# Kernel optimization log

Measured on AMD Instinct MI355X. Metric: run time of the kernel, lower is better.

Reference implementation:

```python
import jax, jax.numpy as jnp
import numpy as np

B, T, C, H, W = 1, 8, 128, 64, 64
F = 64  # num_feat


def setup_inputs() -> dict:
    key = jax.random.key(0)
    ks = jax.random.split(key, 8)
    return {
        "input1": jax.random.normal(ks[0], (B, T, C, H, W), jnp.float32),
        "input2": jax.random.normal(ks[1], (B, T, C, H, W), jnp.float32),
        "W1": jax.random.normal(ks[2], (F, C), jnp.float32) * 0.05,
        "b1": jax.random.normal(ks[3], (F,), jnp.float32) * 0.05,
        "W2": jax.random.normal(ks[4], (F, C), jnp.float32) * 0.05,
        "b2": jax.random.normal(ks[5], (F,), jnp.float32) * 0.05,
        "W3": jax.random.normal(ks[6], (F, C), jnp.float32) * 0.05,
        "b3": jax.random.normal(ks[7], (F,), jnp.float32) * 0.05,
    }


def reference(input1, input2, W1, b1, W2, b2, W3, b3):
    # act == 0 (ReLU branch). Conv1d(kernel=1) == per-position linear projection.
    b, t, c, h, w = input1.shape
    n = h * w
    x1 = input1.reshape(b, t, c, n)  # matches transpose(1,2).reshape then frame slice
    x2 = input2.reshape(b, t, c, n)
    q = jnp.einsum('fc,btcn->btnf', W1, x1) + b1          # [B,T,N,F]
    k = jnp.einsum('fc,btcn->btnf', W2, x2) + b2          # [B,T,N,F]
    g = jnp.einsum('fc,btcn->btnf', W3, x1) + b3          # [B,T,N,F]
    scores = jax.nn.relu(jnp.einsum('btnf,btmf->btnm', q, k))  # [B,T,N,N]
    out = jnp.einsum('btnm,btmf->btnf', scores, g)        # [B,T,N,F]
    # view([B,H,W,F]).permute(0,3,1,2), stacked over T -> [B,T,F,H,W]
    return out.reshape(b, t, h, w, -1).transpose(0, 1, 4, 2, 3)
```

## Files before the change

### kernel.cpp

```cpp
#include <hip/hip_runtime.h>
#include <hip/hip_bf16.h>

constexpr int T = 8;
constexpr int C = 128;
constexpr int N = 4096;
constexpr int F = 64;

typedef __bf16 bf16x8 __attribute__((ext_vector_type(8)));
typedef __bf16 bf16x4 __attribute__((ext_vector_type(4)));
typedef float  f32x4  __attribute__((ext_vector_type(4)));

__global__ __launch_bounds__(256) void proj_kernel(
    const float* __restrict__ x1, const float* __restrict__ x2,
    const float* __restrict__ W1, const float* __restrict__ b1,
    const float* __restrict__ W2, const float* __restrict__ b2,
    const float* __restrict__ W3, const float* __restrict__ b3,
    __bf16* __restrict__ Qb, __bf16* __restrict__ Kb, __bf16* __restrict__ Gw,
    float* __restrict__ out)
{
    const int t   = blockIdx.x >> 6;
    const int nb  = blockIdx.x & 63;
    const int tid = threadIdx.x, wave = tid >> 6, lane = tid & 63;
    const int quad = lane >> 4, l16 = lane & 15;
    const int nw = nb * 64 + wave * 16;

    {
        f32x4* o4 = (f32x4*)out + (size_t)blockIdx.x * 1024;
#pragma unroll
        for (int i = 0; i < 4; ++i) o4[i * 256 + tid] = (f32x4){0.f, 0.f, 0.f, 0.f};
    }

    bf16x8 xf1[4], xf2[4];
#pragma unroll
    for (int cc = 0; cc < 4; ++cc) {
#pragma unroll
        for (int j = 0; j < 8; ++j) {
            size_t off = ((size_t)t * C + cc * 32 + quad * 8 + j) * (size_t)N + nw + l16;
            xf1[cc][j] = (__bf16)x1[off];
            xf2[cc][j] = (__bf16)x2[off];
        }
    }

    const float* Ws[3] = {W1, W2, W3};
    const float* bs[3] = {b1, b2, b3};

#pragma unroll
    for (int p = 0; p < 3; ++p) {
        const float* W    = Ws[p];
        const float* bias = bs[p];
#pragma unroll
        for (int fb = 0; fb < 4; ++fb) {
            f32x4 acc = (f32x4){0.f, 0.f, 0.f, 0.f};
#pragma unroll
            for (int cc = 0; cc < 4; ++cc) {
                const f32x4* wp = (const f32x4*)&W[(fb * 16 + l16) * C + cc * 32 + quad * 8];
                f32x4 w0 = wp[0], w1 = wp[1];
                bf16x8 wf;
                wf[0] = (__bf16)w0[0]; wf[1] = (__bf16)w0[1];
                wf[2] = (__bf16)w0[2]; wf[3] = (__bf16)w0[3];
                wf[4] = (__bf16)w1[0]; wf[5] = (__bf16)w1[1];
                wf[6] = (__bf16)w1[2]; wf[7] = (__bf16)w1[3];
                bf16x8 xb = (p == 1) ? xf2[cc] : xf1[cc];
                acc = __builtin_amdgcn_mfma_f32_16x16x32_bf16(wf, xb, acc, 0, 0, 0);
            }
            if (p < 2) {
                __bf16* O = p ? Kb : Qb;
                bf16x4 ov;
#pragma unroll
                for (int r = 0; r < 4; ++r)
                    ov[r] = (__bf16)(acc[r] + bias[fb * 16 + quad * 4 + r]);
                *(bf16x4*)&O[((size_t)t * N + nw + l16) * F + fb * 16 + quad * 4] = ov;
            } else {
#pragma unroll
                for (int r = 0; r < 4; ++r) {
                    int f = fb * 16 + quad * 4 + r;
                    Gw[((size_t)t * F + f) * (size_t)N + nw + l16] = (__bf16)(acc[r] + bias[f]);
                }
            }
        }
    }
}

constexpr int KSPLIT = 4;

__global__ __launch_bounds__(256) void attn_kernel(
    const __bf16* __restrict__ Qb, const __bf16* __restrict__ Kb,
    const __bf16* __restrict__ Gw, float* __restrict__ out)
{
    const int ks = blockIdx.x & (KSPLIT - 1);
    const int qb = (blockIdx.x / KSPLIT) & 15;
    const int t  = blockIdx.x >> 6;
    const int q0 = qb * 256;

    constexpr int KS = 72;
    __shared__ __bf16 Kt[64 * KS];
    __shared__ __bf16 Gt[64 * KS];
    __shared__ __bf16 Sb[256 * KS];

    const int tid = threadIdx.x, wave = tid >> 6, lane = tid & 63;
    const int quad = lane >> 4, l16 = lane & 15;

    bf16x8 qf[4][2];
#pragma unroll
    for (int qg = 0; qg < 4; ++qg) {
        const __bf16* qrow = &Qb[((size_t)t * N + q0 + wave * 64 + qg * 16 + l16) * F];
        qf[qg][0] = *(const bf16x8*)&qrow[quad * 8];
        qf[qg][1] = *(const bf16x8*)&qrow[32 + quad * 8];
    }

    f32x4 oacc[4][4];
#pragma unroll
    for (int ft = 0; ft < 4; ++ft)
#pragma unroll
        for (int qg = 0; qg < 4; ++qg) oacc[ft][qg] = (f32x4){0.f, 0.f, 0.f, 0.f};

    const int kb_lo = ks * (N / 64 / KSPLIT);
    const int kb_hi = kb_lo + (N / 64 / KSPLIT);

    const int r8a = tid >> 3,          c8a = (tid & 7) * 8;
    const int r8b = (tid + 256) >> 3,  c8b = c8a;

    bf16x8 kv0, kv1, gv0, gv1;
    {
        const int k0 = kb_lo * 64;
        kv0 = *(const bf16x8*)&Kb[((size_t)t * N + k0 + r8a) * F + c8a];
        kv1 = *(const bf16x8*)&Kb[((size_t)t * N + k0 + r8b) * F + c8b];
        gv0 = *(const bf16x8*)&Gw[((size_t)t * F + r8a) * (size_t)N + k0 + c8a];
        gv1 = *(const bf16x8*)&Gw[((size_t)t * F + r8b) * (size_t)N + k0 + c8b];
    }

    for (int kb = kb_lo; kb < kb_hi; ++kb) {
        __syncthreads();
        *(bf16x8*)&Kt[r8a * KS + c8a] = kv0;
        *(bf16x8*)&Kt[r8b * KS + c8b] = kv1;
        *(bf16x8*)&Gt[r8a * KS + c8a] = gv0;
        *(bf16x8*)&Gt[r8b * KS + c8b] = gv1;
        __syncthreads();

        if (kb + 1 < kb_hi) {
            const int k0 = (kb + 1) * 64;
            kv0 = *(const bf16x8*)&Kb[((size_t)t * N + k0 + r8a) * F + c8a];
            kv1 = *(const bf16x8*)&Kb[((size_t)t * N + k0 + r8b) * F + c8b];
            gv0 = *(const bf16x8*)&Gw[((size_t)t * F + r8a) * (size_t)N + k0 + c8a];
            gv1 = *(const bf16x8*)&Gw[((size_t)t * F + r8b) * (size_t)N + k0 + c8b];
        }

#pragma unroll
        for (int nt = 0; nt < 4; ++nt) {
            bf16x8 k0f = *(const bf16x8*)&Kt[(nt * 16 + l16) * KS + quad * 8];
            bf16x8 k1f = *(const bf16x8*)&Kt[(nt * 16 + l16) * KS + 32 + quad * 8];
#pragma unroll
            for (int qg = 0; qg < 4; ++qg) {
                f32x4 s = (f32x4){0.f, 0.f, 0.f, 0.f};
                s = __builtin_amdgcn_mfma_f32_16x16x32_bf16(k0f, qf[qg][0], s, 0, 0, 0);
                s = __builtin_amdgcn_mfma_f32_16x16x32_bf16(k1f, qf[qg][1], s, 0, 0, 0);
                bf16x4 sp;
#pragma unroll
                for (int r = 0; r < 4; ++r) sp[r] = (__bf16)fmaxf(s[r], 0.f);
                *(bf16x4*)&Sb[(wave * 64 + qg * 16 + l16) * KS + nt * 16 + quad * 4] = sp;
            }
        }

        bf16x8 sf[4][2];
#pragma unroll
        for (int qg = 0; qg < 4; ++qg) {
            const __bf16* srow = &Sb[(wave * 64 + qg * 16 + l16) * KS];
            sf[qg][0] = *(const bf16x8*)&srow[quad * 8];
            sf[qg][1] = *(const bf16x8*)&srow[32 + quad * 8];
        }
#pragma unroll
        for (int ft = 0; ft < 4; ++ft) {
            bf16x8 g0 = *(const bf16x8*)&Gt[(ft * 16 + l16) * KS + quad * 8];
            bf16x8 g1 = *(const bf16x8*)&Gt[(ft * 16 + l16) * KS + 32 + quad * 8];
#pragma unroll
            for (int qg = 0; qg < 4; ++qg) {
                oacc[ft][qg] = __builtin_amdgcn_mfma_f32_16x16x32_bf16(g0, sf[qg][0], oacc[ft][qg], 0, 0, 0);
                oacc[ft][qg] = __builtin_amdgcn_mfma_f32_16x16x32_bf16(g1, sf[qg][1], oacc[ft][qg], 0, 0, 0);
            }
        }
    }

#pragma unroll
    for (int ft = 0; ft < 4; ++ft)
#pragma unroll
        for (int qg = 0; qg < 4; ++qg)
#pragma unroll
            for (int r = 0; r < 4; ++r) {
                int f = ft * 16 + quad * 4 + r;
                int q = q0 + wave * 64 + qg * 16 + l16;
                unsafeAtomicAdd(&out[((size_t)t * F + f) * (size_t)N + q], oacc[ft][qg][r]);
            }
}

extern "C" void kernel_launch(void* const* d_in, const int* in_sizes, int n_in,
                              void* d_out, int out_size, void* d_ws, size_t ws_size,
                              hipStream_t stream) {
    const float* x1 = (const float*)d_in[0];
    const float* x2 = (const float*)d_in[1];
    const float* W1 = (const float*)d_in[2];
    const float* b1 = (const float*)d_in[3];
    const float* W2 = (const float*)d_in[4];
    const float* b2 = (const float*)d_in[5];
    const float* W3 = (const float*)d_in[6];
    const float* b3 = (const float*)d_in[7];
    float* out = (float*)d_out;

    __bf16* Qb = (__bf16*)d_ws;
    __bf16* Kb = Qb + (size_t)T * N * F;
    __bf16* Gw = Kb + (size_t)T * N * F;

    proj_kernel<<<dim3(T * (N / 64)), dim3(256), 0, stream>>>(
        x1, x2, W1, b1, W2, b2, W3, b3, Qb, Kb, Gw, out);
    attn_kernel<<<dim3(T * 16 * KSPLIT), dim3(256), 0, stream>>>(Qb, Kb, Gw, out);
}
```

Before: 166.7 us.

## Rewrite attention kernel with 32x32 MFMA, register-resident scores, no LDS

Rewrites the attention kernel around 32x32x16 bf16 MFMAs. Relu'd scores are repacked into B-operand fragments in registers via cross-half-wave shuffles instead of a round trip through shared memory. K and G fragments are now read straight from global memory each iteration, removing LDS staging, the barriers and the explicit prefetch. This cuts LDS traffic and synchronisation, but every wave reloads K/G from global/L2 and loses the software prefetch overlap.

```diff
diff --git a/kernel.cpp b/kernel.cpp
--- a/kernel.cpp
+++ b/kernel.cpp
@@ -9,6 +9,7 @@
 typedef __bf16 bf16x8 __attribute__((ext_vector_type(8)));
 typedef __bf16 bf16x4 __attribute__((ext_vector_type(4)));
 typedef float  f32x4  __attribute__((ext_vector_type(4)));
+typedef float  f32x16 __attribute__((ext_vector_type(16)));
 
 __global__ __launch_bounds__(256) void proj_kernel(
     const float* __restrict__ x1, const float* __restrict__ x2,
@@ -81,6 +82,13 @@
     }
 }
 
+__device__ inline unsigned pk_relu(float a, float b) {
+    union { __bf16 h[2]; unsigned u; } x;
+    x.h[0] = (__bf16)fmaxf(a, 0.f);
+    x.h[1] = (__bf16)fmaxf(b, 0.f);
+    return x.u;
+}
+
 constexpr int KSPLIT = 4;
 
 __global__ __launch_bounds__(256) void attn_kernel(
@@ -89,106 +97,94 @@
 {
     const int ks = blockIdx.x & (KSPLIT - 1);
     const int qb = (blockIdx.x / KSPLIT) & 15;
-    const int t  = blockIdx.x >> 6;
-    const int q0 = qb * 256;
-
-    constexpr int KS = 72;
-    __shared__ __bf16 Kt[64 * KS];
-    __shared__ __bf16 Gt[64 * KS];
-    __shared__ __bf16 Sb[256 * KS];
+    const int t  = blockIdx.x / (KSPLIT * 16);
 
     const int tid = threadIdx.x, wave = tid >> 6, lane = tid & 63;
-    const int quad = lane >> 4, l16 = lane & 15;
-
-    bf16x8 qf[4][2];
-#pragma unroll
-    for (int qg = 0; qg < 4; ++qg) {
-        const __bf16* qrow = &Qb[((size_t)t * N + q0 + wave * 64 + qg * 16 + l16) * F];
-        qf[qg][0] = *(const bf16x8*)&qrow[quad * 8];
-        qf[qg][1] = *(const bf16x8*)&qrow[32 + quad * 8];
-    }
-
-    f32x4 oacc[4][4];
-#pragma unroll
-    for (int ft = 0; ft < 4; ++ft)
-#pragma unroll
-        for (int qg = 0; qg < 4; ++qg) oacc[ft][qg] = (f32x4){0.f, 0.f, 0.f, 0.f};
+    const int l32 = lane & 31, h = lane >> 5;
+    const int qw = qb * 256 + wave * 64;
+
+    const __bf16* Kbase = Kb + (size_t)t * N * F;
+    const __bf16* Gbase = Gw + (size_t)t * F * N;
+
+    bf16x8 qf[2][4];
+#pragma unroll
+    for (int qt = 0; qt < 2; ++qt)
+#pragma unroll
+        for (int c = 0; c < 4; ++c)
+            qf[qt][c] = *(const bf16x8*)&Qb[((size_t)t * N + qw + qt * 32 + l32) * F + c * 16 + h * 8];
+
+    f32x16 oacc[2][2];
+#pragma unroll
+    for (int ft = 0; ft < 2; ++ft)
+#pragma unroll
+        for (int qt = 0; qt < 2; ++qt)
+#pragma unroll
+            for (int i = 0; i < 16; ++i) oacc[ft][qt][i] = 0.f;
 
     const int kb_lo = ks * (N / 64 / KSPLIT);
     const int kb_hi = kb_lo + (N / 64 / KSPLIT);
 
-    const int r8a = tid >> 3,          c8a = (tid & 7) * 8;
-    const int r8b = (tid + 256) >> 3,  c8b = c8a;
-
-    bf16x8 kv0, kv1, gv0, gv1;
-    {
-        const int k0 = kb_lo * 64;
-        kv0 = *(const bf16x8*)&Kb[((size_t)t * N + k0 + r8a) * F + c8a];
-        kv1 = *(const bf16x8*)&Kb[((size_t)t * N + k0 + r8b) * F + c8b];
-        gv0 = *(const bf16x8*)&Gw[((size_t)t * F + r8a) * (size_t)N + k0 + c8a];
-        gv1 = *(const bf16x8*)&Gw[((size_t)t * F + r8b) * (size_t)N + k0 + c8b];
-    }
-
     for (int kb = kb_lo; kb < kb_hi; ++kb) {
-        __syncthreads();
-        *(bf16x8*)&Kt[r8a * KS + c8a] = kv0;
-        *(bf16x8*)&Kt[r8b * KS + c8b] = kv1;
-        *(bf16x8*)&Gt[r8a * KS + c8a] = gv0;
-        *(bf16x8*)&Gt[r8b * KS + c8b] = gv1;
-        __syncthreads();
-
-        if (kb + 1 < kb_hi) {
-            const int k0 = (kb + 1) * 64;
-            kv0 = *(const bf16x8*)&Kb[((size_t)t * N + k0 + r8a) * F + c8a];
-            kv1 = *(const bf16x8*)&Kb[((size_t)t * N + k0 + r8b) * F + c8b];
-            gv0 = *(const bf16x8*)&Gw[((size_t)t * F + r8a) * (size_t)N + k0 + c8a];
-            gv1 = *(const bf16x8*)&Gw[((size_t)t * F + r8b) * (size_t)N + k0 + c8b];
-        }
-
-#pragma unroll
-        for (int nt = 0; nt < 4; ++nt) {
-            bf16x8 k0f = *(const bf16x8*)&Kt[(nt * 16 + l16) * KS + quad * 8];
-            bf16x8 k1f = *(const bf16x8*)&Kt[(nt * 16 + l16) * KS + 32 + quad * 8];
-#pragma unroll
-            for (int qg = 0; qg < 4; ++qg) {
-                f32x4 s = (f32x4){0.f, 0.f, 0.f, 0.f};
-                s = __builtin_amdgcn_mfma_f32_16x16x32_bf16(k0f, qf[qg][0], s, 0, 0, 0);
-                s = __builtin_amdgcn_mfma_f32_16x16x32_bf16(k1f, qf[qg][1], s, 0, 0, 0);
-                bf16x4 sp;
-#pragma unroll
-                for (int r = 0; r < 4; ++r) sp[r] = (__bf16)fmaxf(s[r], 0.f);
-                *(bf16x4*)&Sb[(wave * 64 + qg * 16 + l16) * KS + nt * 16 + quad * 4] = sp;
-            }
-        }
-
-        bf16x8 sf[4][2];
-#pragma unroll
-        for (int qg = 0; qg < 4; ++qg) {
-            const __bf16* srow = &Sb[(wave * 64 + qg * 16 + l16) * KS];
-            sf[qg][0] = *(const bf16x8*)&srow[quad * 8];
-            sf[qg][1] = *(const bf16x8*)&srow[32 + quad * 8];
-        }
-#pragma unroll
-        for (int ft = 0; ft < 4; ++ft) {
-            bf16x8 g0 = *(const bf16x8*)&Gt[(ft * 16 + l16) * KS + quad * 8];
-            bf16x8 g1 = *(const bf16x8*)&Gt[(ft * 16 + l16) * KS + 32 + quad * 8];
-#pragma unroll
-            for (int qg = 0; qg < 4; ++qg) {
-                oacc[ft][qg] = __builtin_amdgcn_mfma_f32_16x16x32_bf16(g0, sf[qg][0], oacc[ft][qg], 0, 0, 0);
-                oacc[ft][qg] = __builtin_amdgcn_mfma_f32_16x16x32_bf16(g1, sf[qg][1], oacc[ft][qg], 0, 0, 0);
-            }
-        }
-    }
-
-#pragma unroll
-    for (int ft = 0; ft < 4; ++ft)
-#pragma unroll
-        for (int qg = 0; qg < 4; ++qg)
-#pragma unroll
-            for (int r = 0; r < 4; ++r) {
-                int f = ft * 16 + quad * 4 + r;
-                int q = q0 + wave * 64 + qg * 16 + l16;
-                unsafeAtomicAdd(&out[((size_t)t * F + f) * (size_t)N + q], oacc[ft][qg][r]);
+        const int k0 = kb * 64;
+        bf16x8 sfrag[2][4];
+
+#pragma unroll
+        for (int kt = 0; kt < 2; ++kt) {
+            f32x16 sd[2];
+#pragma unroll
+            for (int qt = 0; qt < 2; ++qt)
+#pragma unroll
+                for (int i = 0; i < 16; ++i) sd[qt][i] = 0.f;
+#pragma unroll
+            for (int c = 0; c < 4; ++c) {
+                bf16x8 kf = *(const bf16x8*)&Kbase[(size_t)(k0 + kt * 32 + l32) * F + c * 16 + h * 8];
+                sd[0] = __builtin_amdgcn_mfma_f32_32x32x16_bf16(kf, qf[0][c], sd[0], 0, 0, 0);
+                sd[1] = __builtin_amdgcn_mfma_f32_32x32x16_bf16(kf, qf[1][c], sd[1], 0, 0, 0);
+            }
+#pragma unroll
+            for (int qt = 0; qt < 2; ++qt) {
+                unsigned p0 = pk_relu(sd[qt][0],  sd[qt][1]);
+                unsigned p1 = pk_relu(sd[qt][2],  sd[qt][3]);
+                unsigned p2 = pk_relu(sd[qt][4],  sd[qt][5]);
+                unsigned p3 = pk_relu(sd[qt][6],  sd[qt][7]);
+                unsigned p4 = pk_relu(sd[qt][8],  sd[qt][9]);
+                unsigned p5 = pk_relu(sd[qt][10], sd[qt][11]);
+                unsigned p6 = pk_relu(sd[qt][12], sd[qt][13]);
+                unsigned p7 = pk_relu(sd[qt][14], sd[qt][15]);
+                unsigned r0 = (unsigned)__shfl_xor((int)(h ? p0 : p2), 32, 64);
+                unsigned r1 = (unsigned)__shfl_xor((int)(h ? p1 : p3), 32, 64);
+                unsigned r2 = (unsigned)__shfl_xor((int)(h ? p4 : p6), 32, 64);
+                unsigned r3 = (unsigned)__shfl_xor((int)(h ? p5 : p7), 32, 64);
+                union { unsigned u[4]; bf16x8 v; } f0, f1;
+                f0.u[0] = h ? r0 : p0;  f0.u[1] = h ? r1 : p1;
+                f0.u[2] = h ? p2 : r0;  f0.u[3] = h ? p3 : r1;
+                f1.u[0] = h ? r2 : p4;  f1.u[1] = h ? r3 : p5;
+                f1.u[2] = h ? p6 : r2;  f1.u[3] = h ? p7 : r3;
+                sfrag[qt][kt * 2 + 0] = f0.v;
+                sfrag[qt][kt * 2 + 1] = f1.v;
+            }
+        }
+
+#pragma unroll
+        for (int ft = 0; ft < 2; ++ft) {
+#pragma unroll
+            for (int kc = 0; kc < 4; ++kc) {
+                bf16x8 gf = *(const bf16x8*)&Gbase[(size_t)(ft * 32 + l32) * N + k0 + kc * 16 + h * 8];
+                oacc[ft][0] = __builtin_amdgcn_mfma_f32_32x32x16_bf16(gf, sfrag[0][kc], oacc[ft][0], 0, 0, 0);
+                oacc[ft][1] = __builtin_amdgcn_mfma_f32_32x32x16_bf16(gf, sfrag[1][kc], oacc[ft][1], 0, 0, 0);
+            }
+        }
+    }
+
+#pragma unroll
+    for (int ft = 0; ft < 2; ++ft)
+#pragma unroll
+        for (int qt = 0; qt < 2; ++qt)
+#pragma unroll
+            for (int r = 0; r < 16; ++r) {
+                int f = ft * 32 + (r & 3) + 8 * (r >> 2) + 4 * h;
+                int q = qw + qt * 32 + l32;
+                unsafeAtomicAdd(&out[((size_t)t * F + f) * (size_t)N + q], oacc[ft][qt][r]);
             }
 }
 
```

Result: slower. 206.2 us (+23.7%).
